# Kernel tuning notes

Measured on AMD Instinct MI355X. Metric: run time of the kernel, lower is better.

## Reference

```python
import math
import jax, jax.numpy as jnp
import numpy as np

DIM_Q = 1024
DIM_K = 1024
DIM_V = 1024
NUM_HEADS = 16
B, NQ, NK = 4, 1024, 1024
LN_EPS = 1e-5


def setup_inputs() -> dict:
    key = jax.random.key(0)
    ks = jax.random.split(key, 16)
    s = lambda fan_in: 1.0 / math.sqrt(fan_in)
    inp = {
        "Q": jax.random.normal(ks[0], (B, NQ, DIM_Q), dtype=jnp.float32),
        "K": jax.random.normal(ks[1], (B, NK, DIM_K), dtype=jnp.float32),
        # attention projections (nn.Linear: weight [out, in])
        "Wq": jax.random.uniform(ks[2], (DIM_V, DIM_Q), jnp.float32, -s(DIM_Q), s(DIM_Q)),
        "bq": jax.random.uniform(ks[3], (DIM_V,), jnp.float32, -s(DIM_Q), s(DIM_Q)),
        "Wk": jax.random.uniform(ks[4], (DIM_V, DIM_K), jnp.float32, -s(DIM_K), s(DIM_K)),
        "bk": jax.random.uniform(ks[5], (DIM_V,), jnp.float32, -s(DIM_K), s(DIM_K)),
        "Wv": jax.random.uniform(ks[6], (DIM_V, DIM_K), jnp.float32, -s(DIM_K), s(DIM_K)),
        "bv": jax.random.uniform(ks[7], (DIM_V,), jnp.float32, -s(DIM_K), s(DIM_K)),
        # LayerNorms
        "ln0_g": jnp.ones((DIM_V,), jnp.float32),
        "ln0_b": jnp.zeros((DIM_V,), jnp.float32),
        "ln1_g": jnp.ones((DIM_V,), jnp.float32),
        "ln1_b": jnp.zeros((DIM_V,), jnp.float32),
        # SwiGLU: w12 [2*hidden, in], w3 [out, hidden], hidden = out = DIM_V
        "W12": jax.random.uniform(ks[8], (2 * DIM_V, DIM_V), jnp.float32, -s(DIM_V), s(DIM_V)),
        "b12": jax.random.uniform(ks[9], (2 * DIM_V,), jnp.float32, -s(DIM_V), s(DIM_V)),
        "W3": jax.random.uniform(ks[10], (DIM_V, DIM_V), jnp.float32, -s(DIM_V), s(DIM_V)),
        "b3": jax.random.uniform(ks[11], (DIM_V,), jnp.float32, -s(DIM_V), s(DIM_V)),
    }
    return inp


def _layernorm(x, g, b):
    mu = jnp.mean(x, axis=-1, keepdims=True)
    var = jnp.mean(jnp.square(x - mu), axis=-1, keepdims=True)
    return (x - mu) * jax.lax.rsqrt(var + LN_EPS) * g + b


def reference(Q, K, Wq, bq, Wk, bk, Wv, bv, ln0_g, ln0_b, ln1_g, ln1_b, W12, b12, W3, b3):
    H = NUM_HEADS
    dh = DIM_V // H
    Qp = jnp.einsum("bnd,vd->bnv", Q, Wq) + bq   # [B,NQ,DIM_V]
    Kp = jnp.einsum("bnd,vd->bnv", K, Wk) + bk   # [B,NK,DIM_V]
    Vp = jnp.einsum("bnd,vd->bnv", K, Wv) + bv
    # torch.cat(x.split(dh, 2), 0) => layout [H*B, N, dh] with head index major
    Qh = Qp.reshape(B, NQ, H, dh).transpose(2, 0, 1, 3)  # [H,B,NQ,dh]
    Kh = Kp.reshape(B, NK, H, dh).transpose(2, 0, 1, 3)
    Vh = Vp.reshape(B, NK, H, dh).transpose(2, 0, 1, 3)
    # NOTE: original scales by sqrt(dim_V), not sqrt(head_dim)
    scores = jnp.einsum("hbqd,hbkd->hbqk", Qh, Kh) / math.sqrt(DIM_V)
    A = jax.nn.softmax(scores, axis=-1)                  # [H,B,NQ,NK]
    Oh = Qh + jnp.einsum("hbqk,hbkd->hbqd", A, Vh)       # residual pre-concat
    O = Oh.transpose(1, 2, 0, 3).reshape(B, NQ, DIM_V)
    O = _layernorm(O, ln0_g, ln0_b)
    # SwiGLU FFN
    x12 = jnp.einsum("bnd,hd->bnh", O, W12) + b12
    x1, x2 = jnp.split(x12, 2, axis=-1)
    O = O + (jnp.einsum("bnh,oh->bno", jax.nn.silu(x1) * x2, W3) + b3)
    O = _layernorm(O, ln1_g, ln1_b)
    return O, A.reshape(H * B, NQ, NK)
```

## Files before the change

kernel.cpp:

```cpp
#include <hip/hip_runtime.h>
#include <math.h>

#define BATCH 4
#define NQL   1024
#define NKL   1024
#define DIM   1024
#define NHEAD 16
#define DHEAD 64
#define MROWS 4096
#define SCALE 0.03125f

typedef float  f32x4  __attribute__((ext_vector_type(4)));
typedef short  short8 __attribute__((ext_vector_type(8)));

__device__ __forceinline__ ushort f2bf(float x) {
    uint u = __float_as_uint(x);
    u += 0x7FFFu + ((u >> 16) & 1u);
    return (ushort)(u >> 16);
}
__device__ __forceinline__ float bf2f(ushort h) {
    return __uint_as_float(((uint)h) << 16);
}

__global__ __launch_bounds__(256)
void split_bf(const float* __restrict__ x, ushort* __restrict__ hi,
              ushort* __restrict__ lo, int n4)
{
    const int i = blockIdx.x * 256 + threadIdx.x;
    if (i >= n4) return;
    const float4 v = ((const float4*)x)[i];
    ushort4 h, l;
    h.x = f2bf(v.x); l.x = f2bf(v.x - bf2f(h.x));
    h.y = f2bf(v.y); l.y = f2bf(v.y - bf2f(h.y));
    h.z = f2bf(v.z); l.z = f2bf(v.z - bf2f(h.z));
    h.w = f2bf(v.w); l.w = f2bf(v.w - bf2f(h.w));
    ((ushort4*)hi)[i] = h;
    ((ushort4*)lo)[i] = l;
}

template<int NPROD, int BIAS, int RESID, int OUTHI>
__global__ __launch_bounds__(256)
void gemm_mfma(const ushort* __restrict__ Ahi, const ushort* __restrict__ Alo,
               int lda, long aBs, long aHs,
               const ushort* __restrict__ Bhi, const ushort* __restrict__ Blo,
               int ldb, long bBs, long bHs,
               const float* __restrict__ bias,
               const float* __restrict__ rm, long rBs, long rHs,
               float* __restrict__ Cm, ushort* __restrict__ Chi,
               int ldc, long cBs, long cHs,
               int Kd, float scale, int ZB)
{
    constexpr int NT_ = (NPROD == 3) ? 4 : 2;
    __shared__ ushort lds[2][NT_][128 * 32];

    const int tid  = threadIdx.x;
    const int lane = tid & 63;
    const int wid  = tid >> 6;
    const int wr   = wid >> 1, wc = wid & 1;
    const int bm   = blockIdx.x * 128;
    const int bn   = blockIdx.y * 128;

    const int zz = blockIdx.z;
    const int zh = zz / ZB, zb = zz % ZB;
    Ahi += (size_t)zb * aBs + (size_t)zh * aHs;
    Bhi += (size_t)zb * bBs + (size_t)zh * bHs;
    Cm  += (size_t)zb * cBs + (size_t)zh * cHs;
    const float* Rm = nullptr;
    if (RESID) Rm = rm + (size_t)zb * rBs + (size_t)zh * rHs;

    const ushort* tb[NT_];
    int tldv[NT_];
    tb[0] = Ahi + (size_t)bm * lda;  tldv[0] = lda;
    tb[1] = Bhi + (size_t)bn * ldb;  tldv[1] = ldb;
    if constexpr (NPROD == 3) {
        tb[2] = Alo + (size_t)zb * aBs + (size_t)zh * aHs + (size_t)bm * lda;  tldv[2] = lda;
        tb[3] = Blo + (size_t)zb * bBs + (size_t)zh * bHs + (size_t)bn * ldb;  tldv[3] = ldb;
    }

    int4 rg[NT_][2];
    auto gload = [&](int k0) {
#pragma unroll
        for (int tt = 0; tt < NT_; ++tt)
#pragma unroll
            for (int p = 0; p < 2; ++p) {
                const int idx = p * 256 + tid;
                rg[tt][p] = *(const int4*)(tb[tt] + (size_t)(idx >> 2) * tldv[tt]
                                           + k0 + ((idx & 3) << 3));
            }
    };
    auto dswrite = [&](int buf) {
#pragma unroll
        for (int tt = 0; tt < NT_; ++tt)
#pragma unroll
            for (int p = 0; p < 2; ++p)
                *(int4*)&lds[buf][tt][(size_t)(p * 256 + tid) * 8] = rg[tt][p];
    };

    gload(0);
    dswrite(0);
    __syncthreads();

    f32x4 acc[4][4] = {};
    int cur = 0;
    const int nt = Kd >> 5;

    const int rA = wr * 64 + (lane & 15);
    const int rB = wc * 64 + (lane & 15);
    const int kg = (lane >> 4) << 3;

    for (int t = 0; t < nt; ++t) {
        const bool more = (t + 1) < nt;
        if (more) gload((t + 1) << 5);

        short8 ah[4], bh[4], al[4], bl[4];
#pragma unroll
        for (int f = 0; f < 4; ++f) {
            ah[f] = *(const short8*)&lds[cur][0][(size_t)(rA + f * 16) * 32 + kg];
            bh[f] = *(const short8*)&lds[cur][1][(size_t)(rB + f * 16) * 32 + kg];
        }
        if constexpr (NPROD == 3) {
#pragma unroll
            for (int f = 0; f < 4; ++f) {
                al[f] = *(const short8*)&lds[cur][2][(size_t)(rA + f * 16) * 32 + kg];
                bl[f] = *(const short8*)&lds[cur][3][(size_t)(rB + f * 16) * 32 + kg];
            }
        }

#pragma unroll
        for (int fi = 0; fi < 4; ++fi)
#pragma unroll
            for (int fj = 0; fj < 4; ++fj) {
                acc[fi][fj] = __builtin_amdgcn_mfma_f32_16x16x32_bf16(ah[fi], bh[fj], acc[fi][fj], 0, 0, 0);
                if constexpr (NPROD == 3) {
                    acc[fi][fj] = __builtin_amdgcn_mfma_f32_16x16x32_bf16(ah[fi], bl[fj], acc[fi][fj], 0, 0, 0);
                    acc[fi][fj] = __builtin_amdgcn_mfma_f32_16x16x32_bf16(al[fi], bh[fj], acc[fi][fj], 0, 0, 0);
                }
            }

        if (more) dswrite(cur ^ 1);
        __syncthreads();
        cur ^= 1;
    }

    float biasv[4];
    if (BIAS) {
#pragma unroll
        for (int fj = 0; fj < 4; ++fj)
            biasv[fj] = bias[bn + wc * 64 + fj * 16 + (lane & 15)];
    }
#pragma unroll
    for (int fi = 0; fi < 4; ++fi) {
        const int r0 = bm + wr * 64 + fi * 16 + ((lane >> 4) << 2);
#pragma unroll
        for (int fj = 0; fj < 4; ++fj) {
            const int c = bn + wc * 64 + fj * 16 + (lane & 15);
#pragma unroll
            for (int r = 0; r < 4; ++r) {
                float o = acc[fi][fj][r] * scale;
                if (BIAS) o += biasv[fj];
                if (RESID) o += Rm[(size_t)(r0 + r) * ldc + c];
                Cm[(size_t)(r0 + r) * ldc + c] = o;
                if (OUTHI) Chi[(size_t)(r0 + r) * ldc + c] = f2bf(o);
            }
        }
    }
}

#define BT 128
#define LDB2 132

__global__ __launch_bounds__(256)
void fused_smax_pv(float* __restrict__ Aout,
                   const float* __restrict__ Vp,
                   const float* __restrict__ Qp,
                   float* __restrict__ Oa)
{
    __shared__ float As[16][LDB2];
    __shared__ float Bs[16][68];
    __shared__ float sm_m[128], sm_li[128];

    const int tid  = threadIdx.x;
    const int lane = tid & 63;
    const int wv   = tid >> 6;
    const int bm   = blockIdx.x * BT;
    const int z    = blockIdx.z;
    const int zh   = z >> 2, zb = z & 3;

    float* Ab       = Aout + (size_t)z * (1u << 20) + (size_t)bm * NKL;
    const float* Vb = Vp + (size_t)zb * (1u << 20) + (size_t)zh * DHEAD;
    const float* Qb = Qp + (size_t)zb * (1u << 20) + (size_t)zh * DHEAD + (size_t)bm * DIM;
    float* Ob       = Oa + (size_t)zb * (1u << 20) + (size_t)zh * DHEAD + (size_t)bm * DIM;

    for (int r = wv; r < BT; r += 4) {
        const float* p = Ab + (size_t)r * NKL + (lane << 2);
        float4 x0 = *(const float4*)(p);
        float4 x1 = *(const float4*)(p + 256);
        float4 x2 = *(const float4*)(p + 512);
        float4 x3 = *(const float4*)(p + 768);
        float m = fmaxf(fmaxf(fmaxf(x0.x, x0.y), fmaxf(x0.z, x0.w)),
                        fmaxf(fmaxf(x1.x, x1.y), fmaxf(x1.z, x1.w)));
        m = fmaxf(m, fmaxf(fmaxf(fmaxf(x2.x, x2.y), fmaxf(x2.z, x2.w)),
                           fmaxf(fmaxf(x3.x, x3.y), fmaxf(x3.z, x3.w))));
#pragma unroll
        for (int off = 32; off; off >>= 1) m = fmaxf(m, __shfl_xor(m, off));
        float s = __expf(x0.x - m) + __expf(x0.y - m) + __expf(x0.z - m) + __expf(x0.w - m)
                + __expf(x1.x - m) + __expf(x1.y - m) + __expf(x1.z - m) + __expf(x1.w - m)
                + __expf(x2.x - m) + __expf(x2.y - m) + __expf(x2.z - m) + __expf(x2.w - m)
                + __expf(x3.x - m) + __expf(x3.y - m) + __expf(x3.z - m) + __expf(x3.w - m);
#pragma unroll
        for (int off = 32; off; off >>= 1) s += __shfl_xor(s, off);
        if (lane == 0) { sm_m[r] = m; sm_li[r] = 1.f / s; }
    }
    __syncthreads();

    const float m0  = sm_m[tid >> 2],  m1  = sm_m[(tid >> 2) + 64];
    const float li0 = sm_li[tid >> 2], li1 = sm_li[(tid >> 2) + 64];

    const int tx = tid & 15;
    const int ty = tid >> 4;
    const int lrow = tid >> 2;
    const int lk4  = (tid & 3) << 2;
    const int bkk  = tid >> 4;
    const int bn0  = (tid & 15) << 2;

    float acc[8][4] = {};

    float* Ap0 = Ab + (size_t)lrow * NKL + lk4;
    float* Ap1 = Ab + (size_t)(lrow + 64) * NKL + lk4;
    const float* Vpp = Vb + (size_t)bkk * DIM + bn0;

    float4 a0v = *(const float4*)(Ap0);
    float4 a1v = *(const float4*)(Ap1);
    float4 bvv = *(const float4*)(Vpp);

    for (int k0 = 0; k0 < NKL; k0 += 16) {
        float4 p0, p1;
        p0.x = __expf(a0v.x - m0) * li0;  p0.y = __expf(a0v.y - m0) * li0;
        p0.z = __expf(a0v.z - m0) * li0;  p0.w = __expf(a0v.w - m0) * li0;
        p1.x = __expf(a1v.x - m1) * li1;  p1.y = __expf(a1v.y - m1) * li1;
        p1.z = __expf(a1v.z - m1) * li1;  p1.w = __expf(a1v.w - m1) * li1;
        *(float4*)(Ap0 + k0) = p0;
        *(float4*)(Ap1 + k0) = p1;

        __syncthreads();
        As[lk4 + 0][lrow] = p0.x;  As[lk4 + 1][lrow] = p0.y;
        As[lk4 + 2][lrow] = p0.z;  As[lk4 + 3][lrow] = p0.w;
        As[lk4 + 0][lrow + 64] = p1.x;  As[lk4 + 1][lrow + 64] = p1.y;
        As[lk4 + 2][lrow + 64] = p1.z;  As[lk4 + 3][lrow + 64] = p1.w;
        *(float4*)&Bs[bkk][bn0] = bvv;
        __syncthreads();

        if (k0 + 16 < NKL) {
            a0v = *(const float4*)(Ap0 + k0 + 16);
            a1v = *(const float4*)(Ap1 + k0 + 16);
            bvv = *(const float4*)(Vpp + (size_t)(k0 + 16) * DIM);
        }

#pragma unroll
        for (int kk = 0; kk < 16; ++kk) {
            const float4 a0 = *(const float4*)&As[kk][ty << 3];
            const float4 a1 = *(const float4*)&As[kk][(ty << 3) + 4];
            const float4 b  = *(const float4*)&Bs[kk][tx << 2];
            const float aa[8] = {a0.x, a0.y, a0.z, a0.w, a1.x, a1.y, a1.z, a1.w};
            const float bb[4] = {b.x, b.y, b.z, b.w};
#pragma unroll
            for (int i = 0; i < 8; ++i)
#pragma unroll
                for (int j = 0; j < 4; ++j)
                    acc[i][j] = fmaf(aa[i], bb[j], acc[i][j]);
        }
    }

#pragma unroll
    for (int i = 0; i < 8; ++i) {
        const size_t idx = (size_t)((ty << 3) + i) * DIM + (tx << 2);
        const float4 q = *(const float4*)(Qb + idx);
        float4 v = make_float4(acc[i][0] + q.x, acc[i][1] + q.y,
                               acc[i][2] + q.z, acc[i][3] + q.w);
        *(float4*)(Ob + idx) = v;
    }
}

template<int SPLIT>
__global__ __launch_bounds__(256)
void ln_rows(const float* __restrict__ in, const float* __restrict__ g,
             const float* __restrict__ b, float* __restrict__ out,
             ushort* __restrict__ ohi, ushort* __restrict__ olo)
{
    const int row = blockIdx.x;
    const int tid = threadIdx.x;
    const float4 xv = *(const float4*)(in + (size_t)row * DIM + (tid << 2));

    float s = xv.x + xv.y + xv.z + xv.w;
    float q = xv.x * xv.x + xv.y * xv.y + xv.z * xv.z + xv.w * xv.w;
#pragma unroll
    for (int off = 32; off; off >>= 1) {
        s += __shfl_xor(s, off);
        q += __shfl_xor(q, off);
    }
    __shared__ float ss[4], qq[4];
    if ((tid & 63) == 0) { ss[tid >> 6] = s; qq[tid >> 6] = q; }
    __syncthreads();
    s = ss[0] + ss[1] + ss[2] + ss[3];
    q = qq[0] + qq[1] + qq[2] + qq[3];

    const float mu  = s * (1.f / 1024.f);
    const float var = q * (1.f / 1024.f) - mu * mu;
    const float rs  = rsqrtf(var + 1e-5f);

    const float4 gv = *(const float4*)(g + (tid << 2));
    const float4 bv = *(const float4*)(b + (tid << 2));
    float4 o;
    o.x = (xv.x - mu) * rs * gv.x + bv.x;
    o.y = (xv.y - mu) * rs * gv.y + bv.y;
    o.z = (xv.z - mu) * rs * gv.z + bv.z;
    o.w = (xv.w - mu) * rs * gv.w + bv.w;
    *(float4*)(out + (size_t)row * DIM + (tid << 2)) = o;

    if (SPLIT) {
        ushort4 h, l;
        h.x = f2bf(o.x); l.x = f2bf(o.x - bf2f(h.x));
        h.y = f2bf(o.y); l.y = f2bf(o.y - bf2f(h.y));
        h.z = f2bf(o.z); l.z = f2bf(o.z - bf2f(h.z));
        h.w = f2bf(o.w); l.w = f2bf(o.w - bf2f(h.w));
        ((ushort4*)(ohi + (size_t)row * DIM))[tid] = h;
        ((ushort4*)(olo + (size_t)row * DIM))[tid] = l;
    }
}

__global__ __launch_bounds__(256)
void silu_mul(const float* __restrict__ x12, ushort* __restrict__ ghi,
              ushort* __restrict__ glo)
{
    const int i = blockIdx.x * 256 + threadIdx.x;
    const int n = i >> 8;
    const int c = (i & 255) << 2;
    const float4 a = *(const float4*)(x12 + (size_t)n * 2048 + c);
    const float4 b = *(const float4*)(x12 + (size_t)n * 2048 + 1024 + c);
    float4 o;
    o.x = a.x / (1.f + __expf(-a.x)) * b.x;
    o.y = a.y / (1.f + __expf(-a.y)) * b.y;
    o.z = a.z / (1.f + __expf(-a.z)) * b.z;
    o.w = a.w / (1.f + __expf(-a.w)) * b.w;
    ushort4 h, l;
    h.x = f2bf(o.x); l.x = f2bf(o.x - bf2f(h.x));
    h.y = f2bf(o.y); l.y = f2bf(o.y - bf2f(h.y));
    h.z = f2bf(o.z); l.z = f2bf(o.z - bf2f(h.z));
    h.w = f2bf(o.w); l.w = f2bf(o.w - bf2f(h.w));
    ((ushort4*)ghi)[i] = h;
    ((ushort4*)glo)[i] = l;
}

extern "C" void kernel_launch(void* const* d_in, const int* in_sizes, int n_in,
                              void* d_out, int out_size, void* d_ws, size_t ws_size,
                              hipStream_t stream)
{
    const float* Q   = (const float*)d_in[0];
    const float* K   = (const float*)d_in[1];
    const float* Wq  = (const float*)d_in[2];
    const float* bq  = (const float*)d_in[3];
    const float* Wk  = (const float*)d_in[4];
    const float* bk  = (const float*)d_in[5];
    const float* Wv  = (const float*)d_in[6];
    const float* bv  = (const float*)d_in[7];
    const float* g0  = (const float*)d_in[8];
    const float* be0 = (const float*)d_in[9];
    const float* g1  = (const float*)d_in[10];
    const float* be1 = (const float*)d_in[11];
    const float* W12 = (const float*)d_in[12];
    const float* b12 = (const float*)d_in[13];
    const float* W3  = (const float*)d_in[14];
    const float* b3  = (const float*)d_in[15];

    float* ws   = (float*)d_ws;
    float* Qp   = ws;
    float* Kp   = ws + (1u << 22);
    float* Vp   = ws + (2u << 22);
    float* Oa   = ws + (3u << 22);
    float* Oln  = ws + (4u << 22);
    float* x12  = ws;

    ushort* u     = (ushort*)(ws + (5u << 22));
    ushort* QpHi  = u;
    ushort* KpHi  = u + (1u << 22);
    ushort* Qhi   = u + (2u << 22);
    ushort* Qlo   = u + (3u << 22);
    ushort* Khi   = u + (4u << 22);
    ushort* Klo   = u + (5u << 22);
    ushort* OlnHi = Qhi;
    ushort* OlnLo = Qlo;
    ushort* GHi   = Khi;
    ushort* GLo   = Klo;
    ushort* Wqhi  = u + (6u << 22);
    ushort* Wqlo  = Wqhi + (1u << 20);
    ushort* Wkhi  = Wqhi + (2u << 20);
    ushort* Wklo  = Wqhi + (3u << 20);
    ushort* Wvhi  = Wqhi + (4u << 20);
    ushort* Wvlo  = Wqhi + (5u << 20);
    ushort* W12hi = Wqhi + (6u << 20);
    ushort* W12lo = Wqhi + (8u << 20);
    ushort* W3hi  = Wqhi + (10u << 20);
    ushort* W3lo  = Wqhi + (11u << 20);

    float* Oout = (float*)d_out;
    float* Aout = Oout + (1u << 22);

    const dim3 blk(256);
    const long MB1 = 1L << 20;
    const long MB4 = 4L << 20;

    split_bf<<<4096, blk, 0, stream>>>(Q,   Qhi,   Qlo,   1 << 20);
    split_bf<<<4096, blk, 0, stream>>>(K,   Khi,   Klo,   1 << 20);
    split_bf<<<1024, blk, 0, stream>>>(Wq,  Wqhi,  Wqlo,  1 << 18);
    split_bf<<<1024, blk, 0, stream>>>(Wk,  Wkhi,  Wklo,  1 << 18);
    split_bf<<<1024, blk, 0, stream>>>(Wv,  Wvhi,  Wvlo,  1 << 18);
    split_bf<<<2048, blk, 0, stream>>>(W12, W12hi, W12lo, 1 << 19);
    split_bf<<<1024, blk, 0, stream>>>(W3,  W3hi,  W3lo,  1 << 18);

    gemm_mfma<3,1,0,1><<<dim3(32,8,1), blk, 0, stream>>>(
        Qhi, Qlo, DIM, 0,0, Wqhi, Wqlo, DIM, 0,0, bq,
        nullptr, 0,0, Qp, QpHi, DIM, 0,0, DIM, 1.f, 1);
    gemm_mfma<3,1,0,1><<<dim3(32,8,1), blk, 0, stream>>>(
        Khi, Klo, DIM, 0,0, Wkhi, Wklo, DIM, 0,0, bk,
        nullptr, 0,0, Kp, KpHi, DIM, 0,0, DIM, 1.f, 1);
    gemm_mfma<3,1,0,0><<<dim3(32,8,1), blk, 0, stream>>>(
        Khi, Klo, DIM, 0,0, Wvhi, Wvlo, DIM, 0,0, bv,
        nullptr, 0,0, Vp, nullptr, DIM, 0,0, DIM, 1.f, 1);

    gemm_mfma<1,0,0,0><<<dim3(8,8,64), blk, 0, stream>>>(
        QpHi, nullptr, DIM, MB1, (long)DHEAD, KpHi, nullptr, DIM, MB1, (long)DHEAD,
        nullptr, nullptr, 0,0, Aout, nullptr, NKL, MB1, MB4, DHEAD, SCALE, BATCH);

    fused_smax_pv<<<dim3(8,1,64), blk, 0, stream>>>(Aout, Vp, Qp, Oa);

    ln_rows<1><<<4096, blk, 0, stream>>>(Oa, g0, be0, Oln, OlnHi, OlnLo);

    gemm_mfma<3,1,0,0><<<dim3(32,16,1), blk, 0, stream>>>(
        OlnHi, OlnLo, DIM, 0,0, W12hi, W12lo, DIM, 0,0, b12,
        nullptr, 0,0, x12, nullptr, 2048, 0,0, DIM, 1.f, 1);

    silu_mul<<<4096, blk, 0, stream>>>(x12, GHi, GLo);

    gemm_mfma<3,1,1,0><<<dim3(32,8,1), blk, 0, stream>>>(
        GHi, GLo, DIM, 0,0, W3hi, W3lo, DIM, 0,0, b3,
        Oln, 0,0, Oa, nullptr, DIM, 0,0, DIM, 1.f, 1);

    ln_rows<0><<<4096, blk, 0, stream>>>(Oa, g1, be1, Oout, nullptr, nullptr);
}
```

Baseline: 1.165 ms.

## Replace score GEMM and softmax-PV kernels with fused two-pass flash attention

The separate QK^T GEMM, which wrote fp32 scores to the attention output, and the softmax+PV kernel that reread them are replaced by one flash-style kernel. It makes a first pass over K to get row max and sum, then a second pass that recomputes scores, writes the normalized probabilities once and does P·V with bf16 MFMA. The V projection now writes a bf16 head-transposed layout directly, and the GEMM LDS tiles are padded to a stride of 40 to cut bank conflicts. This removes a full fp32 read-modify-write of the 64M-element attention matrix in exchange for computing QK^T twice, and the P·V product now runs in bf16 instead of fp32 FMA.

```diff
diff --git a/kernel.cpp b/kernel.cpp
--- a/kernel.cpp
+++ b/kernel.cpp
@@ -7,7 +7,6 @@
 #define DIM   1024
 #define NHEAD 16
 #define DHEAD 64
-#define MROWS 4096
 #define SCALE 0.03125f
 
 typedef float  f32x4  __attribute__((ext_vector_type(4)));
@@ -38,20 +37,21 @@
     ((ushort4*)lo)[i] = l;
 }
 
-template<int NPROD, int BIAS, int RESID, int OUTHI>
+#define LDK 40
+
+template<int NPROD, int BIAS, int RESID, int OMODE>
 __global__ __launch_bounds__(256)
 void gemm_mfma(const ushort* __restrict__ Ahi, const ushort* __restrict__ Alo,
-               int lda, long aBs, long aHs,
+               int lda,
                const ushort* __restrict__ Bhi, const ushort* __restrict__ Blo,
-               int ldb, long bBs, long bHs,
+               int ldb,
                const float* __restrict__ bias,
-               const float* __restrict__ rm, long rBs, long rHs,
+               const float* __restrict__ rm,
                float* __restrict__ Cm, ushort* __restrict__ Chi,
-               int ldc, long cBs, long cHs,
-               int Kd, float scale, int ZB)
+               int ldc, int Kd, float scale)
 {
     constexpr int NT_ = (NPROD == 3) ? 4 : 2;
-    __shared__ ushort lds[2][NT_][128 * 32];
+    __shared__ ushort lds[2][NT_][128 * LDK];
 
     const int tid  = threadIdx.x;
     const int lane = tid & 63;
@@ -60,21 +60,13 @@
     const int bm   = blockIdx.x * 128;
     const int bn   = blockIdx.y * 128;
 
-    const int zz = blockIdx.z;
-    const int zh = zz / ZB, zb = zz % ZB;
-    Ahi += (size_t)zb * aBs + (size_t)zh * aHs;
-    Bhi += (size_t)zb * bBs + (size_t)zh * bHs;
-    Cm  += (size_t)zb * cBs + (size_t)zh * cHs;
-    const float* Rm = nullptr;
-    if (RESID) Rm = rm + (size_t)zb * rBs + (size_t)zh * rHs;
-
     const ushort* tb[NT_];
     int tldv[NT_];
     tb[0] = Ahi + (size_t)bm * lda;  tldv[0] = lda;
     tb[1] = Bhi + (size_t)bn * ldb;  tldv[1] = ldb;
     if constexpr (NPROD == 3) {
-        tb[2] = Alo + (size_t)zb * aBs + (size_t)zh * aHs + (size_t)bm * lda;  tldv[2] = lda;
-        tb[3] = Blo + (size_t)zb * bBs + (size_t)zh * bHs + (size_t)bn * ldb;  tldv[3] = ldb;
+        tb[2] = Alo + (size_t)bm * lda;  tldv[2] = lda;
+        tb[3] = Blo + (size_t)bn * ldb;  tldv[3] = ldb;
     }
 
     int4 rg[NT_][2];
@@ -92,8 +84,10 @@
 #pragma unroll
         for (int tt = 0; tt < NT_; ++tt)
 #pragma unroll
-            for (int p = 0; p < 2; ++p)
-                *(int4*)&lds[buf][tt][(size_t)(p * 256 + tid) * 8] = rg[tt][p];
+            for (int p = 0; p < 2; ++p) {
+                const int idx = p * 256 + tid;
+                *(int4*)&lds[buf][tt][(idx >> 2) * LDK + ((idx & 3) << 3)] = rg[tt][p];
+            }
     };
 
     gload(0);
@@ -115,14 +109,14 @@
         short8 ah[4], bh[4], al[4], bl[4];
 #pragma unroll
         for (int f = 0; f < 4; ++f) {
-            ah[f] = *(const short8*)&lds[cur][0][(size_t)(rA + f * 16) * 32 + kg];
-            bh[f] = *(const short8*)&lds[cur][1][(size_t)(rB + f * 16) * 32 + kg];
+            ah[f] = *(const short8*)&lds[cur][0][(rA + f * 16) * LDK + kg];
+            bh[f] = *(const short8*)&lds[cur][1][(rB + f * 16) * LDK + kg];
         }
         if constexpr (NPROD == 3) {
 #pragma unroll
             for (int f = 0; f < 4; ++f) {
-                al[f] = *(const short8*)&lds[cur][2][(size_t)(rA + f * 16) * 32 + kg];
-                bl[f] = *(const short8*)&lds[cur][3][(size_t)(rB + f * 16) * 32 + kg];
+                al[f] = *(const short8*)&lds[cur][2][(rA + f * 16) * LDK + kg];
+                bl[f] = *(const short8*)&lds[cur][3][(rB + f * 16) * LDK + kg];
             }
         }
 
@@ -154,131 +148,217 @@
 #pragma unroll
         for (int fj = 0; fj < 4; ++fj) {
             const int c = bn + wc * 64 + fj * 16 + (lane & 15);
-#pragma unroll
-            for (int r = 0; r < 4; ++r) {
-                float o = acc[fi][fj][r] * scale;
-                if (BIAS) o += biasv[fj];
-                if (RESID) o += Rm[(size_t)(r0 + r) * ldc + c];
-                Cm[(size_t)(r0 + r) * ldc + c] = o;
-                if (OUTHI) Chi[(size_t)(r0 + r) * ldc + c] = f2bf(o);
-            }
-        }
-    }
-}
-
-#define BT 128
-#define LDB2 132
+            if constexpr (OMODE == 3) {
+                ushort4 v4;
+#pragma unroll
+                for (int r = 0; r < 4; ++r) {
+                    float o = acc[fi][fj][r] * scale;
+                    if (BIAS) o += biasv[fj];
+                    ((ushort*)&v4)[r] = f2bf(o);
+                }
+                const int b   = r0 >> 10;
+                const int key = r0 & 1023;
+                const int h   = c >> 6;
+                const int d   = c & 63;
+                *(ushort4*)(Chi + ((size_t)((h << 2) + b) << 16) + (size_t)d * 1024 + key) = v4;
+            } else {
+#pragma unroll
+                for (int r = 0; r < 4; ++r) {
+                    float o = acc[fi][fj][r] * scale;
+                    if (BIAS) o += biasv[fj];
+                    if (RESID) o += rm[(size_t)(r0 + r) * ldc + c];
+                    if (OMODE == 0 || OMODE == 1)
+                        Cm[(size_t)(r0 + r) * ldc + c] = o;
+                    if (OMODE == 1 || OMODE == 2)
+                        Chi[(size_t)(r0 + r) * ldc + c] = f2bf(o);
+                }
+            }
+        }
+    }
+}
 
 __global__ __launch_bounds__(256)
-void fused_smax_pv(float* __restrict__ Aout,
-                   const float* __restrict__ Vp,
-                   const float* __restrict__ Qp,
-                   float* __restrict__ Oa)
+void flash_attn(const ushort* __restrict__ QpHi,
+                const ushort* __restrict__ KpHi,
+                const ushort* __restrict__ Vt,
+                const float*  __restrict__ Qp,
+                float* __restrict__ Aout,
+                float* __restrict__ Oa)
 {
-    __shared__ float As[16][LDB2];
-    __shared__ float Bs[16][68];
-    __shared__ float sm_m[128], sm_li[128];
+    __shared__ ushort Ks[2][64][72];
+    __shared__ ushort Vs[2][64][72];
+    __shared__ ushort Ps[4][32][72];
 
     const int tid  = threadIdx.x;
     const int lane = tid & 63;
-    const int wv   = tid >> 6;
-    const int bm   = blockIdx.x * BT;
-    const int z    = blockIdx.z;
-    const int zh   = z >> 2, zb = z & 3;
-
-    float* Ab       = Aout + (size_t)z * (1u << 20) + (size_t)bm * NKL;
-    const float* Vb = Vp + (size_t)zb * (1u << 20) + (size_t)zh * DHEAD;
-    const float* Qb = Qp + (size_t)zb * (1u << 20) + (size_t)zh * DHEAD + (size_t)bm * DIM;
-    float* Ob       = Oa + (size_t)zb * (1u << 20) + (size_t)zh * DHEAD + (size_t)bm * DIM;
-
-    for (int r = wv; r < BT; r += 4) {
-        const float* p = Ab + (size_t)r * NKL + (lane << 2);
-        float4 x0 = *(const float4*)(p);
-        float4 x1 = *(const float4*)(p + 256);
-        float4 x2 = *(const float4*)(p + 512);
-        float4 x3 = *(const float4*)(p + 768);
-        float m = fmaxf(fmaxf(fmaxf(x0.x, x0.y), fmaxf(x0.z, x0.w)),
-                        fmaxf(fmaxf(x1.x, x1.y), fmaxf(x1.z, x1.w)));
-        m = fmaxf(m, fmaxf(fmaxf(fmaxf(x2.x, x2.y), fmaxf(x2.z, x2.w)),
-                           fmaxf(fmaxf(x3.x, x3.y), fmaxf(x3.z, x3.w))));
-#pragma unroll
-        for (int off = 32; off; off >>= 1) m = fmaxf(m, __shfl_xor(m, off));
-        float s = __expf(x0.x - m) + __expf(x0.y - m) + __expf(x0.z - m) + __expf(x0.w - m)
-                + __expf(x1.x - m) + __expf(x1.y - m) + __expf(x1.z - m) + __expf(x1.w - m)
-                + __expf(x2.x - m) + __expf(x2.y - m) + __expf(x2.z - m) + __expf(x2.w - m)
-                + __expf(x3.x - m) + __expf(x3.y - m) + __expf(x3.z - m) + __expf(x3.w - m);
-#pragma unroll
-        for (int off = 32; off; off >>= 1) s += __shfl_xor(s, off);
-        if (lane == 0) { sm_m[r] = m; sm_li[r] = 1.f / s; }
-    }
+    const int w    = tid >> 6;
+    const int l15  = lane & 15;
+    const int lg   = lane >> 4;
+    const int bm   = blockIdx.x * 128;
+    const int hb   = blockIdx.y;
+    const int zh   = hb >> 2, zb = hb & 3;
+
+    const ushort* Qb  = QpHi + ((size_t)zb << 20) + zh * 64;
+    const ushort* Kb  = KpHi + ((size_t)zb << 20) + zh * 64;
+    const ushort* Vtb = Vt   + ((size_t)hb << 16);
+    const float*  Qrb = Qp   + ((size_t)zb << 20) + zh * 64 + (size_t)bm * DIM;
+    float* Ab = Aout + ((size_t)hb << 20) + (size_t)bm * NKL;
+    float* Ob = Oa   + ((size_t)zb << 20) + zh * 64 + (size_t)bm * DIM;
+
+    short8 qf[2][2];
+#pragma unroll
+    for (int qg = 0; qg < 2; ++qg)
+#pragma unroll
+        for (int kg = 0; kg < 2; ++kg)
+            qf[qg][kg] = *(const short8*)(Qb + (size_t)(bm + w * 32 + qg * 16 + l15) * DIM
+                                          + kg * 32 + lg * 8);
+
+    int4 kreg[2], vreg[2];
+    auto kload = [&](int kt) {
+#pragma unroll
+        for (int p = 0; p < 2; ++p) {
+            const int c = p * 256 + tid;
+            kreg[p] = *(const int4*)(Kb + (size_t)(kt * 64 + (c >> 3)) * DIM + (c & 7) * 8);
+        }
+    };
+    auto kstore = [&](int buf) {
+#pragma unroll
+        for (int p = 0; p < 2; ++p) {
+            const int c = p * 256 + tid;
+            *(int4*)&Ks[buf][c >> 3][(c & 7) * 8] = kreg[p];
+        }
+    };
+    auto vload = [&](int kt) {
+#pragma unroll
+        for (int p = 0; p < 2; ++p) {
+            const int c = p * 256 + tid;
+            vreg[p] = *(const int4*)(Vtb + (size_t)(c >> 3) * 1024 + kt * 64 + (c & 7) * 8);
+        }
+    };
+    auto vstore = [&](int buf) {
+#pragma unroll
+        for (int p = 0; p < 2; ++p) {
+            const int c = p * 256 + tid;
+            *(int4*)&Vs[buf][c >> 3][(c & 7) * 8] = vreg[p];
+        }
+    };
+    auto qk = [&](int buf, f32x4 (*s)[4]) {
+        short8 kf[4][2];
+#pragma unroll
+        for (int cg = 0; cg < 4; ++cg)
+#pragma unroll
+            for (int kg = 0; kg < 2; ++kg)
+                kf[cg][kg] = *(const short8*)&Ks[buf][cg * 16 + l15][kg * 32 + lg * 8];
+#pragma unroll
+        for (int qg = 0; qg < 2; ++qg)
+#pragma unroll
+            for (int cg = 0; cg < 4; ++cg) {
+                s[qg][cg] = __builtin_amdgcn_mfma_f32_16x16x32_bf16(qf[qg][0], kf[cg][0], s[qg][cg], 0, 0, 0);
+                s[qg][cg] = __builtin_amdgcn_mfma_f32_16x16x32_bf16(qf[qg][1], kf[cg][1], s[qg][cg], 0, 0, 0);
+            }
+    };
+
+    float mrun[2][4], lrun[2][4];
+#pragma unroll
+    for (int qg = 0; qg < 2; ++qg)
+#pragma unroll
+        for (int r = 0; r < 4; ++r) { mrun[qg][r] = -INFINITY; lrun[qg][r] = 0.f; }
+
+    kload(0); kstore(0); __syncthreads();
+    for (int kt = 0; kt < 16; ++kt) {
+        const bool more = kt < 15;
+        if (more) kload(kt + 1);
+        f32x4 s[2][4] = {};
+        qk(kt & 1, s);
+#pragma unroll
+        for (int qg = 0; qg < 2; ++qg)
+#pragma unroll
+            for (int r = 0; r < 4; ++r) {
+                const float v0 = s[qg][0][r] * SCALE, v1 = s[qg][1][r] * SCALE;
+                const float v2 = s[qg][2][r] * SCALE, v3 = s[qg][3][r] * SCALE;
+                const float tm = fmaxf(fmaxf(v0, v1), fmaxf(v2, v3));
+                const float mn = fmaxf(mrun[qg][r], tm);
+                const float sc = __expf(mrun[qg][r] - mn);
+                lrun[qg][r] = lrun[qg][r] * sc
+                            + __expf(v0 - mn) + __expf(v1 - mn)
+                            + __expf(v2 - mn) + __expf(v3 - mn);
+                mrun[qg][r] = mn;
+            }
+        if (more) { kstore((kt + 1) & 1); __syncthreads(); }
+    }
+
+    float mf[2][4], li[2][4];
+#pragma unroll
+    for (int qg = 0; qg < 2; ++qg)
+#pragma unroll
+        for (int r = 0; r < 4; ++r) {
+            float m = mrun[qg][r];
+#pragma unroll
+            for (int off = 1; off < 16; off <<= 1) m = fmaxf(m, __shfl_xor(m, off));
+            float lv = lrun[qg][r] * __expf(mrun[qg][r] - m);
+#pragma unroll
+            for (int off = 1; off < 16; off <<= 1) lv += __shfl_xor(lv, off);
+            mf[qg][r] = m;
+            li[qg][r] = 1.f / lv;
+        }
+
+    kload(0); vload(0);
     __syncthreads();
-
-    const float m0  = sm_m[tid >> 2],  m1  = sm_m[(tid >> 2) + 64];
-    const float li0 = sm_li[tid >> 2], li1 = sm_li[(tid >> 2) + 64];
-
-    const int tx = tid & 15;
-    const int ty = tid >> 4;
-    const int lrow = tid >> 2;
-    const int lk4  = (tid & 3) << 2;
-    const int bkk  = tid >> 4;
-    const int bn0  = (tid & 15) << 2;
-
-    float acc[8][4] = {};
-
-    float* Ap0 = Ab + (size_t)lrow * NKL + lk4;
-    float* Ap1 = Ab + (size_t)(lrow + 64) * NKL + lk4;
-    const float* Vpp = Vb + (size_t)bkk * DIM + bn0;
-
-    float4 a0v = *(const float4*)(Ap0);
-    float4 a1v = *(const float4*)(Ap1);
-    float4 bvv = *(const float4*)(Vpp);
-
-    for (int k0 = 0; k0 < NKL; k0 += 16) {
-        float4 p0, p1;
-        p0.x = __expf(a0v.x - m0) * li0;  p0.y = __expf(a0v.y - m0) * li0;
-        p0.z = __expf(a0v.z - m0) * li0;  p0.w = __expf(a0v.w - m0) * li0;
-        p1.x = __expf(a1v.x - m1) * li1;  p1.y = __expf(a1v.y - m1) * li1;
-        p1.z = __expf(a1v.z - m1) * li1;  p1.w = __expf(a1v.w - m1) * li1;
-        *(float4*)(Ap0 + k0) = p0;
-        *(float4*)(Ap1 + k0) = p1;
-
-        __syncthreads();
-        As[lk4 + 0][lrow] = p0.x;  As[lk4 + 1][lrow] = p0.y;
-        As[lk4 + 2][lrow] = p0.z;  As[lk4 + 3][lrow] = p0.w;
-        As[lk4 + 0][lrow + 64] = p1.x;  As[lk4 + 1][lrow + 64] = p1.y;
-        As[lk4 + 2][lrow + 64] = p1.z;  As[lk4 + 3][lrow + 64] = p1.w;
-        *(float4*)&Bs[bkk][bn0] = bvv;
-        __syncthreads();
-
-        if (k0 + 16 < NKL) {
-            a0v = *(const float4*)(Ap0 + k0 + 16);
-            a1v = *(const float4*)(Ap1 + k0 + 16);
-            bvv = *(const float4*)(Vpp + (size_t)(k0 + 16) * DIM);
-        }
-
-#pragma unroll
-        for (int kk = 0; kk < 16; ++kk) {
-            const float4 a0 = *(const float4*)&As[kk][ty << 3];
-            const float4 a1 = *(const float4*)&As[kk][(ty << 3) + 4];
-            const float4 b  = *(const float4*)&Bs[kk][tx << 2];
-            const float aa[8] = {a0.x, a0.y, a0.z, a0.w, a1.x, a1.y, a1.z, a1.w};
-            const float bb[4] = {b.x, b.y, b.z, b.w};
-#pragma unroll
-            for (int i = 0; i < 8; ++i)
-#pragma unroll
-                for (int j = 0; j < 4; ++j)
-                    acc[i][j] = fmaf(aa[i], bb[j], acc[i][j]);
-        }
-    }
-
-#pragma unroll
-    for (int i = 0; i < 8; ++i) {
-        const size_t idx = (size_t)((ty << 3) + i) * DIM + (tx << 2);
-        const float4 q = *(const float4*)(Qb + idx);
-        float4 v = make_float4(acc[i][0] + q.x, acc[i][1] + q.y,
-                               acc[i][2] + q.z, acc[i][3] + q.w);
-        *(float4*)(Ob + idx) = v;
-    }
+    kstore(0); vstore(0);
+    __syncthreads();
+
+    f32x4 oacc[2][4] = {};
+    for (int kt = 0; kt < 16; ++kt) {
+        const bool more = kt < 15;
+        if (more) { kload(kt + 1); vload(kt + 1); }
+        f32x4 s[2][4] = {};
+        qk(kt & 1, s);
+
+#pragma unroll
+        for (int qg = 0; qg < 2; ++qg)
+#pragma unroll
+            for (int cg = 0; cg < 4; ++cg) {
+#pragma unroll
+                for (int r = 0; r < 4; ++r) {
+                    const float p = __expf(s[qg][cg][r] * SCALE - mf[qg][r]) * li[qg][r];
+                    Ps[w][qg * 16 + lg * 4 + r][cg * 16 + l15] = f2bf(p);
+                    Ab[(size_t)(w * 32 + qg * 16 + lg * 4 + r) * NKL
+                       + kt * 64 + cg * 16 + l15] = p;
+                }
+            }
+
+        short8 pf[2][2], vf[4][2];
+#pragma unroll
+        for (int qg = 0; qg < 2; ++qg)
+#pragma unroll
+            for (int kk = 0; kk < 2; ++kk)
+                pf[qg][kk] = *(const short8*)&Ps[w][qg * 16 + l15][kk * 32 + lg * 8];
+#pragma unroll
+        for (int dg = 0; dg < 4; ++dg)
+#pragma unroll
+            for (int kk = 0; kk < 2; ++kk)
+                vf[dg][kk] = *(const short8*)&Vs[kt & 1][dg * 16 + l15][kk * 32 + lg * 8];
+#pragma unroll
+        for (int qg = 0; qg < 2; ++qg)
+#pragma unroll
+            for (int dg = 0; dg < 4; ++dg) {
+                oacc[qg][dg] = __builtin_amdgcn_mfma_f32_16x16x32_bf16(pf[qg][0], vf[dg][0], oacc[qg][dg], 0, 0, 0);
+                oacc[qg][dg] = __builtin_amdgcn_mfma_f32_16x16x32_bf16(pf[qg][1], vf[dg][1], oacc[qg][dg], 0, 0, 0);
+            }
+
+        if (more) { kstore((kt + 1) & 1); vstore((kt + 1) & 1); __syncthreads(); }
+    }
+
+#pragma unroll
+    for (int qg = 0; qg < 2; ++qg)
+#pragma unroll
+        for (int dg = 0; dg < 4; ++dg)
+#pragma unroll
+            for (int r = 0; r < 4; ++r) {
+                const size_t idx = (size_t)(w * 32 + qg * 16 + lg * 4 + r) * DIM
+                                 + dg * 16 + l15;
+                Ob[idx] = oacc[qg][dg][r] + Qrb[idx];
+            }
 }
 
 template<int SPLIT>
@@ -374,11 +454,17 @@
 
     float* ws   = (float*)d_ws;
     float* Qp   = ws;
-    float* Kp   = ws + (1u << 22);
-    float* Vp   = ws + (2u << 22);
-    float* Oa   = ws + (3u << 22);
-    float* Oln  = ws + (4u << 22);
-    float* x12  = ws;
+    float* Oa   = ws + (1u << 22);
+    float* Oln  = ws + (2u << 22);
+    float* x12  = ws + (3u << 22);
+
+    ushort* wsm   = (ushort*)(ws + (3u << 22));
+    ushort* Wqhi  = wsm;
+    ushort* Wqlo  = wsm + (1u << 20);
+    ushort* Wkhi  = wsm + (2u << 20);
+    ushort* Wklo  = wsm + (3u << 20);
+    ushort* Wvhi  = wsm + (4u << 20);
+    ushort* Wvlo  = wsm + (5u << 20);
 
     ushort* u     = (ushort*)(ws + (5u << 22));
     ushort* QpHi  = u;
@@ -387,27 +473,20 @@
     ushort* Qlo   = u + (3u << 22);
     ushort* Khi   = u + (4u << 22);
     ushort* Klo   = u + (5u << 22);
+    ushort* Vt    = u + (6u << 22);
     ushort* OlnHi = Qhi;
     ushort* OlnLo = Qlo;
     ushort* GHi   = Khi;
     ushort* GLo   = Klo;
-    ushort* Wqhi  = u + (6u << 22);
-    ushort* Wqlo  = Wqhi + (1u << 20);
-    ushort* Wkhi  = Wqhi + (2u << 20);
-    ushort* Wklo  = Wqhi + (3u << 20);
-    ushort* Wvhi  = Wqhi + (4u << 20);
-    ushort* Wvlo  = Wqhi + (5u << 20);
-    ushort* W12hi = Wqhi + (6u << 20);
-    ushort* W12lo = Wqhi + (8u << 20);
-    ushort* W3hi  = Wqhi + (10u << 20);
-    ushort* W3lo  = Wqhi + (11u << 20);
+    ushort* W12hi = u + (7u << 22);
+    ushort* W12lo = W12hi + (1u << 21);
+    ushort* W3hi  = W12hi + (2u << 21);
+    ushort* W3lo  = W12hi + (3u << 21);
 
     float* Oout = (float*)d_out;
     float* Aout = Oout + (1u << 22);
 
     const dim3 blk(256);
-    const long MB1 = 1L << 20;
-    const long MB4 = 4L << 20;
 
     split_bf<<<4096, blk, 0, stream>>>(Q,   Qhi,   Qlo,   1 << 20);
     split_bf<<<4096, blk, 0, stream>>>(K,   Khi,   Klo,   1 << 20);
@@ -417,33 +496,24 @@
     split_bf<<<2048, blk, 0, stream>>>(W12, W12hi, W12lo, 1 << 19);
     split_bf<<<1024, blk, 0, stream>>>(W3,  W3hi,  W3lo,  1 << 18);
 
-    gemm_mfma<3,1,0,1><<<dim3(32,8,1), blk, 0, stream>>>(
-        Qhi, Qlo, DIM, 0,0, Wqhi, Wqlo, DIM, 0,0, bq,
-        nullptr, 0,0, Qp, QpHi, DIM, 0,0, DIM, 1.f, 1);
-    gemm_mfma<3,1,0,1><<<dim3(32,8,1), blk, 0, stream>>>(
-        Khi, Klo, DIM, 0,0, Wkhi, Wklo, DIM, 0,0, bk,
-        nullptr, 0,0, Kp, KpHi, DIM, 0,0, DIM, 1.f, 1);
-    gemm_mfma<3,1,0,0><<<dim3(32,8,1), blk, 0, stream>>>(
-        Khi, Klo, DIM, 0,0, Wvhi, Wvlo, DIM, 0,0, bv,
-        nullptr, 0,0, Vp, nullptr, DIM, 0,0, DIM, 1.f, 1);
-
-    gemm_mfma<1,0,0,0><<<dim3(8,8,64), blk, 0, stream>>>(
-        QpHi, nullptr, DIM, MB1, (long)DHEAD, KpHi, nullptr, DIM, MB1, (long)DHEAD,
-        nullptr, nullptr, 0,0, Aout, nullptr, NKL, MB1, MB4, DHEAD, SCALE, BATCH);
-
-    fused_smax_pv<<<dim3(8,1,64), blk, 0, stream>>>(Aout, Vp, Qp, Oa);
+    gemm_mfma<3,1,0,1><<<dim3(32,8), blk, 0, stream>>>(
+        Qhi, Qlo, DIM, Wqhi, Wqlo, DIM, bq, nullptr, Qp, QpHi, DIM, DIM, 1.f);
+    gemm_mfma<3,1,0,2><<<dim3(32,8), blk, 0, stream>>>(
+        Khi, Klo, DIM, Wkhi, Wklo, DIM, bk, nullptr, nullptr, KpHi, DIM, DIM, 1.f);
+    gemm_mfma<3,1,0,3><<<dim3(32,8), blk, 0, stream>>>(
+        Khi, Klo, DIM, Wvhi, Wvlo, DIM, bv, nullptr, nullptr, Vt, DIM, DIM, 1.f);
+
+    flash_attn<<<dim3(8,64), blk, 0, stream>>>(QpHi, KpHi, Vt, Qp, Aout, Oa);
 
     ln_rows<1><<<4096, blk, 0, stream>>>(Oa, g0, be0, Oln, OlnHi, OlnLo);
 
-    gemm_mfma<3,1,0,0><<<dim3(32,16,1), blk, 0, stream>>>(
-        OlnHi, OlnLo, DIM, 0,0, W12hi, W12lo, DIM, 0,0, b12,
-        nullptr, 0,0, x12, nullptr, 2048, 0,0, DIM, 1.f, 1);
+    gemm_mfma<3,1,0,0><<<dim3(32,16), blk, 0, stream>>>(
+        OlnHi, OlnLo, DIM, W12hi, W12lo, DIM, b12, nullptr, x12, nullptr, 2048, DIM, 1.f);
 
     silu_mul<<<4096, blk, 0, stream>>>(x12, GHi, GLo);
 
-    gemm_mfma<3,1,1,0><<<dim3(32,8,1), blk, 0, stream>>>(
-        GHi, GLo, DIM, 0,0, W3hi, W3lo, DIM, 0,0, b3,
-        Oln, 0,0, Oa, nullptr, DIM, 0,0, DIM, 1.f, 1);
+    gemm_mfma<3,1,1,0><<<dim3(32,8), blk, 0, stream>>>(
+        GHi, GLo, DIM, W3hi, W3lo, DIM, b3, Oln, Oa, nullptr, DIM, DIM, 1.f);
 
     ln_rows<0><<<4096, blk, 0, stream>>>(Oa, g1, be1, Oout, nullptr, nullptr);
 }
```

New measurement: 979.3 us. -16.0%, faster.
